# Optimization experiments

Measured on AMD Instinct MI355X. Metric: run time of the kernel, lower is better.

The kernel has to match this reference:

```python
import jax, jax.numpy as jnp
import numpy as np

N_HEAD = 8
EPS = 1e-5


def setup_inputs() -> dict:
    key = jax.random.key(0)
    ks = jax.random.split(key, 8)
    B, Nq, Ns, C, D = 4, 2048, 2048, 256, 256
    k = jax.random.normal(ks[0], (B, Ns, C), dtype=jnp.float32)
    v = jax.random.normal(ks[1], (B, Ns, D), dtype=jnp.float32)
    q = jax.random.normal(ks[2], (B, Nq, C), dtype=jnp.float32)
    idt = jax.random.normal(ks[3], (B, Nq, D), dtype=jnp.float32)
    s_valid_mask = jax.random.randint(ks[4], (B, Ns), 0, 2, dtype=jnp.int32)
    W_qk = jax.random.normal(ks[5], (C, C), dtype=jnp.float32) / np.sqrt(C)
    W_fc = jax.random.normal(ks[6], (D, D), dtype=jnp.float32) / np.sqrt(D)
    b_fc = jnp.zeros((D,), dtype=jnp.float32)
    ln_w = jnp.ones((D,), dtype=jnp.float32)
    ln_b = jnp.zeros((D,), dtype=jnp.float32)
    return {"k": k, "v": v, "q": q, "idt": idt, "s_valid_mask": s_valid_mask,
            "W_qk": W_qk, "W_fc": W_fc, "b_fc": b_fc, "ln_w": ln_w, "ln_b": ln_b}


def reference(k, v, q, idt, s_valid_mask, W_qk, W_fc, b_fc, ln_w, ln_b):
    B, Nq, C = q.shape
    Ns, D = v.shape[1], v.shape[2]
    H = N_HEAD
    hd = C // H
    temp = hd ** (-0.5)
    # shared qk projection (Linear, no bias): y = x @ W^T
    qh = (q @ W_qk.T).reshape(B, Nq, H, hd)  # bqhd
    kh = (k @ W_qk.T).reshape(B, Ns, H, hd)  # bkhd
    vh = v.reshape(B, Ns, H, D // H)         # bkhd (v_fc is Identity)
    scores = jnp.einsum('bqhd,bkhd->bhqk', qh, kh) * temp
    # additive padding mask: masked (==1) positions get -1000
    mask = s_valid_mask.astype(scores.dtype)[:, None, None, :] * (-1000.0)
    attn = jax.nn.softmax(scores + mask, axis=-1)  # (B,H,Nq,Ns)
    out = jnp.einsum('bhqk,bkhd->bqhd', attn, vh).reshape(B, Nq, D)
    out = out @ W_fc.T + b_fc
    x = out + idt
    mu = jnp.mean(x, axis=-1, keepdims=True)
    var = jnp.mean((x - mu) ** 2, axis=-1, keepdims=True)
    out_ln = (x - mu) * jax.lax.rsqrt(var + EPS) * ln_w + ln_b
    return out_ln, attn.reshape(B * H, Nq, Ns)
```

## Files before the change

### kernel.cpp

```cpp
#include <hip/hip_runtime.h>
#include <hip/hip_bf16.h>

typedef __bf16 bf16;
typedef __attribute__((ext_vector_type(8))) __bf16 b16x8;
typedef __attribute__((ext_vector_type(4))) float f32x4;
typedef __attribute__((ext_vector_type(4))) int i32x4;

#define MFMA16(a, b, c) __builtin_amdgcn_mfma_f32_16x16x32_bf16((a), (b), (c), 0, 0, 0)

#define QSCALE 0.25501568077324936f
#define MCONST -1442.6950408889634f

__global__ void __launch_bounds__(256) k_prep(const float* __restrict__ q,
                                              const float* __restrict__ kk,
                                              const float* __restrict__ Wqk,
                                              const float* __restrict__ v,
                                              const float* __restrict__ Wfc,
                                              const int* __restrict__ svalid,
                                              bf16* __restrict__ ph,
                                              bf16* __restrict__ vT,
                                              bf16* __restrict__ Wfcb,
                                              float* __restrict__ maskf) {
    __shared__ __align__(16) char smem[10240];
    int tid = threadIdx.x;
    int idx = blockIdx.x;
    if (idx < 1024) {
        bf16(*sA)[40] = (bf16(*)[40])smem;
        bf16(*sB)[40] = (bf16(*)[40])(smem + 5120);
        int w = tid >> 6, l = tid & 63, lg = l >> 4, ll = l & 15;
        int wm = w >> 1, wn = w & 1;
        int m0 = (idx & 255) * 64, n0 = (idx >> 8) * 64;
        const float* A = (m0 < 8192) ? q + (size_t)m0 * 256 : kk + (size_t)(m0 - 8192) * 256;
        float osc = (m0 < 8192) ? QSCALE : 1.0f;
        f32x4 acc[2][2] = {};
        int ar = tid >> 2, ac = (tid & 3) * 8;
#pragma unroll
        for (int k0 = 0; k0 < 256; k0 += 32) {
            __syncthreads();
            f32x4 a0 = *(const f32x4*)(A + (size_t)ar * 256 + k0 + ac);
            f32x4 a1 = *(const f32x4*)(A + (size_t)ar * 256 + k0 + ac + 4);
            f32x4 b0 = *(const f32x4*)(Wqk + (size_t)(n0 + ar) * 256 + k0 + ac);
            f32x4 b1 = *(const f32x4*)(Wqk + (size_t)(n0 + ar) * 256 + k0 + ac + 4);
            b16x8 av, bv;
#pragma unroll
            for (int i = 0; i < 4; i++) {
                av[i] = (bf16)a0[i]; av[4 + i] = (bf16)a1[i];
                bv[i] = (bf16)b0[i]; bv[4 + i] = (bf16)b1[i];
            }
            *(b16x8*)&sA[ar][ac] = av;
            *(b16x8*)&sB[ar][ac] = bv;
            __syncthreads();
            b16x8 af[2], bfr[2];
#pragma unroll
            for (int f = 0; f < 2; f++) {
                af[f] = *(b16x8*)&sA[wm * 32 + f * 16 + ll][8 * lg];
                bfr[f] = *(b16x8*)&sB[wn * 32 + f * 16 + ll][8 * lg];
            }
#pragma unroll
            for (int i = 0; i < 2; i++)
#pragma unroll
                for (int j = 0; j < 2; j++) acc[i][j] = MFMA16(af[i], bfr[j], acc[i][j]);
        }
#pragma unroll
        for (int i = 0; i < 2; i++)
#pragma unroll
            for (int j = 0; j < 2; j++) {
                int row = m0 + wm * 32 + i * 16 + lg * 4;
                int col = n0 + wn * 32 + j * 16 + ll;
#pragma unroll
                for (int r = 0; r < 4; r++)
                    ph[(size_t)(row + r) * 256 + col] = (bf16)(acc[i][j][r] * osc);
            }
    } else if (idx < 2048) {
        bf16(*sT)[72] = (bf16(*)[72])smem;
        int i2 = idx - 1024;
        int bh = i2 >> 5, b = bh >> 3, h = bh & 7;
        int ns0 = (i2 & 31) * 64;
        int ns = tid >> 2;
        int dp = (tid & 3) * 8;
        const float* sp = v + ((size_t)(b * 2048 + ns0 + ns)) * 256 + h * 32 + dp;
        f32x4 a = *(const f32x4*)sp;
        f32x4 c = *(const f32x4*)(sp + 4);
#pragma unroll
        for (int i = 0; i < 4; i++) sT[dp + i][ns] = (bf16)a[i];
#pragma unroll
        for (int i = 0; i < 4; i++) sT[dp + 4 + i][ns] = (bf16)c[i];
        __syncthreads();
        int d = tid >> 3;
        int nc = (tid & 7) * 8;
        b16x8 o = *(b16x8*)&sT[d][nc];
        *(b16x8*)(vT + ((size_t)bh * 32 + d) * 2048 + ns0 + nc) = o;
    } else if (idx < 2080) {
        int i = (idx - 2048) * 2048 + tid * 8;
        f32x4 a = *(const f32x4*)(Wfc + i);
        f32x4 b = *(const f32x4*)(Wfc + i + 4);
        b16x8 o;
        o[0] = (bf16)a[0]; o[1] = (bf16)a[1]; o[2] = (bf16)a[2]; o[3] = (bf16)a[3];
        o[4] = (bf16)b[0]; o[5] = (bf16)b[1]; o[6] = (bf16)b[2]; o[7] = (bf16)b[3];
        *(b16x8*)(Wfcb + i) = o;
    } else {
#pragma unroll
        for (int c = 0; c < 32; c++) {
            int i = c * 256 + tid;
            maskf[i] = MCONST * (float)svalid[i];
        }
    }
}

__global__ void __launch_bounds__(256) k_attn(const bf16* __restrict__ ph,
                                              const bf16* __restrict__ vT,
                                              const float* __restrict__ maskf,
                                              bf16* __restrict__ xO,
                                              float* __restrict__ attn) {
    __shared__ __align__(16) bf16 sK[64][40];
    __shared__ __align__(16) bf16 sV[32][72];
    __shared__ __align__(16) float sPf[4][16][68];
    int tid = threadIdx.x;
    int w = tid >> 6, l = tid & 63, lg = l >> 4, ll = l & 15;
    int bh = blockIdx.x >> 5, qt = blockIdx.x & 31;
    int b = bh >> 3, h = bh & 7;
    int qrow0 = qt * 64 + w * 16;
    b16x8 qf = *(const b16x8*)(ph + (size_t)(b * 2048 + qrow0 + ll) * 256 + h * 32 + 8 * lg);
    const float* mrow = maskf + b * 2048;
    const bf16* kbase = ph + (size_t)(8192 + b * 2048) * 256 + h * 32;
    const bf16* vbase = vT + (size_t)(bh * 32) * 2048;
    int kr = tid >> 2, kc = (tid & 3) * 8;
    int dr = tid >> 3, nc2 = (tid & 7) * 8;
    float lsum = 0.f;
    {
        *(b16x8*)&sK[kr][kc] = *(const b16x8*)(kbase + (size_t)kr * 256 + kc);
        __syncthreads();
        for (int kt = 0; kt < 2048; kt += 64) {
            bool more = (kt + 64) < 2048;
            b16x8 kst;
            if (more)
                kst = *(const b16x8*)(kbase + (size_t)(kt + 64 + kr) * 256 + kc);
            b16x8 kf[4];
#pragma unroll
            for (int n = 0; n < 4; n++) kf[n] = *(b16x8*)&sK[n * 16 + ll][8 * lg];
            f32x4 s[4];
#pragma unroll
            for (int n = 0; n < 4; n++) {
                f32x4 z = {};
                s[n] = MFMA16(kf[n], qf, z);
            }
#pragma unroll
            for (int n = 0; n < 4; n++) {
                f32x4 mk = *(const f32x4*)&mrow[kt + n * 16 + lg * 4];
#pragma unroll
                for (int r = 0; r < 4; r++) lsum += exp2f(s[n][r] + mk[r]);
            }
            __syncthreads();
            if (more) *(b16x8*)&sK[kr][kc] = kst;
            __syncthreads();
        }
    }
    lsum += __shfl_xor(lsum, 16, 64);
    lsum += __shfl_xor(lsum, 32, 64);
    float linv = 1.f / lsum;
    f32x4 o[2] = {};
    float* outb = attn + (size_t)(bh * 2048 + qrow0) * 2048;
    *(b16x8*)&sK[kr][kc] = *(const b16x8*)(kbase + (size_t)kr * 256 + kc);
    *(b16x8*)&sV[dr][nc2] = *(const b16x8*)(vbase + (size_t)dr * 2048 + nc2);
    __syncthreads();
    for (int kt = 0; kt < 2048; kt += 64) {
        bool more = (kt + 64) < 2048;
        b16x8 kst, vst;
        if (more) {
            kst = *(const b16x8*)(kbase + (size_t)(kt + 64 + kr) * 256 + kc);
            vst = *(const b16x8*)(vbase + (size_t)dr * 2048 + kt + 64 + nc2);
        }
        b16x8 kf[4], vf[2][2];
#pragma unroll
        for (int n = 0; n < 4; n++) kf[n] = *(b16x8*)&sK[n * 16 + ll][8 * lg];
#pragma unroll
        for (int ks = 0; ks < 2; ks++)
#pragma unroll
            for (int j = 0; j < 2; j++)
                vf[ks][j] = *(b16x8*)&sV[j * 16 + ll][ks * 32 + 8 * lg];
        f32x4 s[4];
#pragma unroll
        for (int n = 0; n < 4; n++) {
            f32x4 z = {};
            s[n] = MFMA16(kf[n], qf, z);
        }
#pragma unroll
        for (int n = 0; n < 4; n++) {
            f32x4 mk = *(const f32x4*)&mrow[kt + n * 16 + lg * 4];
            f32x4 ov;
#pragma unroll
            for (int r = 0; r < 4; r++) ov[r] = exp2f(s[n][r] + mk[r]) * linv;
            *(f32x4*)&sPf[w][ll][n * 16 + lg * 4] = ov;
        }
#pragma unroll
        for (int j = 0; j < 4; j++) {
            int row16 = lg + 4 * j;
            f32x4 v = *(f32x4*)&sPf[w][row16][ll * 4];
            __builtin_nontemporal_store(v, (f32x4*)(outb + (size_t)row16 * 2048 + kt + ll * 4));
        }
#pragma unroll
        for (int ks = 0; ks < 2; ks++) {
            f32x4 p0 = *(f32x4*)&sPf[w][ll][ks * 32 + 8 * lg];
            f32x4 p1 = *(f32x4*)&sPf[w][ll][ks * 32 + 8 * lg + 4];
            b16x8 pf;
#pragma unroll
            for (int i = 0; i < 4; i++) {
                pf[i] = (bf16)p0[i];
                pf[4 + i] = (bf16)p1[i];
            }
#pragma unroll
            for (int j = 0; j < 2; j++) o[j] = MFMA16(pf, vf[ks][j], o[j]);
        }
        __syncthreads();
        if (more) {
            *(b16x8*)&sK[kr][kc] = kst;
            *(b16x8*)&sV[dr][nc2] = vst;
        }
        __syncthreads();
    }
#pragma unroll
    for (int r = 0; r < 4; r++) {
        int row = b * 2048 + qrow0 + lg * 4 + r;
#pragma unroll
        for (int j = 0; j < 2; j++) {
            int col = h * 32 + j * 16 + ll;
            xO[(size_t)(row >> 5) * 16384 + (row & 31) * 256 + col] = (bf16)o[j][r];
        }
    }
}

__global__ void __launch_bounds__(256) k_fcln(const bf16* __restrict__ xO,
                                              const bf16* __restrict__ Wfcb,
                                              const float* __restrict__ bias,
                                              const float* __restrict__ idt,
                                              const float* __restrict__ lnw,
                                              const float* __restrict__ lnb,
                                              float* __restrict__ out) {
    __shared__ __align__(16) bf16 sA[32][264];
    __shared__ __align__(16) bf16 sB[256][40];
    __shared__ float sRed[4][32][2];
    int tid = threadIdx.x;
    int w = tid >> 6, l = tid & 63, lg = l >> 4, ll = l & 15;
    int t = blockIdx.x;
#pragma unroll
    for (int c = 0; c < 4; c++) {
        int col = (tid & 7) * 8 + c * 64;
        *(b16x8*)&sA[tid >> 3][col] =
            *(const b16x8*)(xO + (size_t)t * 16384 + (tid >> 3) * 256 + col);
    }
    __syncthreads();
    f32x4 acc[2][4] = {};
#pragma unroll
    for (int k0 = 0; k0 < 256; k0 += 32) {
        if (k0) __syncthreads();
#pragma unroll
        for (int c = 0; c < 4; c++)
            *(b16x8*)&sB[tid][c * 8] = *(const b16x8*)(Wfcb + (size_t)tid * 256 + k0 + c * 8);
        __syncthreads();
        b16x8 af[2];
#pragma unroll
        for (int i = 0; i < 2; i++) af[i] = *(b16x8*)&sA[i * 16 + ll][k0 + 8 * lg];
#pragma unroll
        for (int j = 0; j < 4; j++) {
            b16x8 bfr = *(b16x8*)&sB[w * 64 + j * 16 + ll][8 * lg];
#pragma unroll
            for (int i = 0; i < 2; i++) acc[i][j] = MFMA16(af[i], bfr, acc[i][j]);
        }
    }
    float bcol[4], wcol[4], bbl[4];
#pragma unroll
    for (int j = 0; j < 4; j++) {
        int col = w * 64 + j * 16 + ll;
        bcol[j] = bias[col];
        wcol[j] = lnw[col];
        bbl[j] = lnb[col];
    }
#pragma unroll
    for (int i = 0; i < 2; i++)
#pragma unroll
        for (int r = 0; r < 4; r++) {
            int row32 = i * 16 + lg * 4 + r;
            int grow = t * 32 + row32;
            float a = 0.f, b2 = 0.f;
#pragma unroll
            for (int j = 0; j < 4; j++) {
                float xv = acc[i][j][r] + bcol[j] + idt[(size_t)grow * 256 + w * 64 + j * 16 + ll];
                acc[i][j][r] = xv;
                a += xv;
                b2 += xv * xv;
            }
#pragma unroll
            for (int off = 1; off < 16; off <<= 1) {
                a += __shfl_xor(a, off, 64);
                b2 += __shfl_xor(b2, off, 64);
            }
            if (ll == 0) {
                sRed[w][row32][0] = a;
                sRed[w][row32][1] = b2;
            }
        }
    __syncthreads();
#pragma unroll
    for (int i = 0; i < 2; i++)
#pragma unroll
        for (int r = 0; r < 4; r++) {
            int row32 = i * 16 + lg * 4 + r;
            int grow = t * 32 + row32;
            float st = sRed[0][row32][0] + sRed[1][row32][0] + sRed[2][row32][0] + sRed[3][row32][0];
            float st2 = sRed[0][row32][1] + sRed[1][row32][1] + sRed[2][row32][1] + sRed[3][row32][1];
            float mu = st * (1.f / 256.f);
            float var = st2 * (1.f / 256.f) - mu * mu;
            float rstd = rsqrtf(var + 1e-5f);
#pragma unroll
            for (int j = 0; j < 4; j++)
                out[(size_t)grow * 256 + w * 64 + j * 16 + ll] =
                    (acc[i][j][r] - mu) * rstd * wcol[j] + bbl[j];
        }
}

extern "C" void kernel_launch(void* const* d_in, const int* in_sizes, int n_in,
                              void* d_out, int out_size, void* d_ws, size_t ws_size,
                              hipStream_t stream) {
    const float* k_in = (const float*)d_in[0];
    const float* v_in = (const float*)d_in[1];
    const float* q_in = (const float*)d_in[2];
    const float* idt  = (const float*)d_in[3];
    const int* svalid = (const int*)d_in[4];
    const float* Wqk  = (const float*)d_in[5];
    const float* Wfc  = (const float*)d_in[6];
    const float* bfc  = (const float*)d_in[7];
    const float* lnw  = (const float*)d_in[8];
    const float* lnb  = (const float*)d_in[9];

    float* out_ln = (float*)d_out;
    float* attn = out_ln + 2097152;

    char* ws = (char*)d_ws;
    bf16* ph     = (bf16*)ws;
    bf16* vT     = (bf16*)(ws + 8388608);
    bf16* Wfcb   = (bf16*)(ws + 12582912);
    float* maskf = (float*)(ws + 12713984);

    bf16* xO = (bf16*)out_ln;

    k_prep<<<2081, 256, 0, stream>>>(q_in, k_in, Wqk, v_in, Wfc, svalid, ph, vT, Wfcb, maskf);
    k_attn<<<1024, 256, 0, stream>>>(ph, vT, maskf, xO, attn);
    k_fcln<<<256, 256, 0, stream>>>(xO, Wfcb, bfc, idt, lnw, lnb, out_ln);
}
```

Baseline: 183.2 us.

## Load K and V fragments directly from global into registers, drop LDS staging

The attention kernel stops staging K and V tiles through shared memory. Each wave now loads its own MFMA operand fragments straight from global memory into registers and prefetches the next tile one iteration ahead. This removes both block-wide barriers per iteration and the LDS round trip. In exchange each K/V element is fetched by all four waves instead of once per block, which relies on cache hits, and the extra prefetch registers raise register pressure.

```diff
diff --git a/kernel.cpp b/kernel.cpp
--- a/kernel.cpp
+++ b/kernel.cpp
@@ -112,8 +112,6 @@
                                               const float* __restrict__ maskf,
                                               bf16* __restrict__ xO,
                                               float* __restrict__ attn) {
-    __shared__ __align__(16) bf16 sK[64][40];
-    __shared__ __align__(16) bf16 sV[32][72];
     __shared__ __align__(16) float sPf[4][16][68];
     int tid = threadIdx.x;
     int w = tid >> 6, l = tid & 63, lg = l >> 4, ll = l & 15;
@@ -122,22 +120,21 @@
     int qrow0 = qt * 64 + w * 16;
     b16x8 qf = *(const b16x8*)(ph + (size_t)(b * 2048 + qrow0 + ll) * 256 + h * 32 + 8 * lg);
     const float* mrow = maskf + b * 2048;
-    const bf16* kbase = ph + (size_t)(8192 + b * 2048) * 256 + h * 32;
-    const bf16* vbase = vT + (size_t)(bh * 32) * 2048;
-    int kr = tid >> 2, kc = (tid & 3) * 8;
-    int dr = tid >> 3, nc2 = (tid & 7) * 8;
+    const bf16* kfb = ph + (size_t)(8192 + b * 2048) * 256 + h * 32 + 8 * lg;
+    const bf16* vfb = vT + (size_t)(bh * 32) * 2048 + 8 * lg;
     float lsum = 0.f;
     {
-        *(b16x8*)&sK[kr][kc] = *(const b16x8*)(kbase + (size_t)kr * 256 + kc);
-        __syncthreads();
+        b16x8 kf[4], kn[4];
+#pragma unroll
+        for (int n = 0; n < 4; n++)
+            kf[n] = *(const b16x8*)(kfb + (size_t)(n * 16 + ll) * 256);
         for (int kt = 0; kt < 2048; kt += 64) {
             bool more = (kt + 64) < 2048;
-            b16x8 kst;
-            if (more)
-                kst = *(const b16x8*)(kbase + (size_t)(kt + 64 + kr) * 256 + kc);
-            b16x8 kf[4];
-#pragma unroll
-            for (int n = 0; n < 4; n++) kf[n] = *(b16x8*)&sK[n * 16 + ll][8 * lg];
+            if (more) {
+#pragma unroll
+                for (int n = 0; n < 4; n++)
+                    kn[n] = *(const b16x8*)(kfb + (size_t)(kt + 64 + n * 16 + ll) * 256);
+            }
             f32x4 s[4];
 #pragma unroll
             for (int n = 0; n < 4; n++) {
@@ -150,9 +147,8 @@
 #pragma unroll
                 for (int r = 0; r < 4; r++) lsum += exp2f(s[n][r] + mk[r]);
             }
-            __syncthreads();
-            if (more) *(b16x8*)&sK[kr][kc] = kst;
-            __syncthreads();
+#pragma unroll
+            for (int n = 0; n < 4; n++) kf[n] = kn[n];
         }
     }
     lsum += __shfl_xor(lsum, 16, 64);
@@ -160,24 +156,27 @@
     float linv = 1.f / lsum;
     f32x4 o[2] = {};
     float* outb = attn + (size_t)(bh * 2048 + qrow0) * 2048;
-    *(b16x8*)&sK[kr][kc] = *(const b16x8*)(kbase + (size_t)kr * 256 + kc);
-    *(b16x8*)&sV[dr][nc2] = *(const b16x8*)(vbase + (size_t)dr * 2048 + nc2);
-    __syncthreads();
+    b16x8 kf[4], kn[4], vf[2][2], vn[2][2];
+#pragma unroll
+    for (int n = 0; n < 4; n++)
+        kf[n] = *(const b16x8*)(kfb + (size_t)(n * 16 + ll) * 256);
+#pragma unroll
+    for (int ks = 0; ks < 2; ks++)
+#pragma unroll
+        for (int j = 0; j < 2; j++)
+            vf[ks][j] = *(const b16x8*)(vfb + (size_t)(j * 16 + ll) * 2048 + ks * 32);
     for (int kt = 0; kt < 2048; kt += 64) {
         bool more = (kt + 64) < 2048;
-        b16x8 kst, vst;
         if (more) {
-            kst = *(const b16x8*)(kbase + (size_t)(kt + 64 + kr) * 256 + kc);
-            vst = *(const b16x8*)(vbase + (size_t)dr * 2048 + kt + 64 + nc2);
-        }
-        b16x8 kf[4], vf[2][2];
-#pragma unroll
-        for (int n = 0; n < 4; n++) kf[n] = *(b16x8*)&sK[n * 16 + ll][8 * lg];
-#pragma unroll
-        for (int ks = 0; ks < 2; ks++)
-#pragma unroll
-            for (int j = 0; j < 2; j++)
-                vf[ks][j] = *(b16x8*)&sV[j * 16 + ll][ks * 32 + 8 * lg];
+#pragma unroll
+            for (int n = 0; n < 4; n++)
+                kn[n] = *(const b16x8*)(kfb + (size_t)(kt + 64 + n * 16 + ll) * 256);
+#pragma unroll
+            for (int ks = 0; ks < 2; ks++)
+#pragma unroll
+                for (int j = 0; j < 2; j++)
+                    vn[ks][j] = *(const b16x8*)(vfb + (size_t)(j * 16 + ll) * 2048 + kt + 64 + ks * 32);
+        }
         f32x4 s[4];
 #pragma unroll
         for (int n = 0; n < 4; n++) {
@@ -211,12 +210,14 @@
 #pragma unroll
             for (int j = 0; j < 2; j++) o[j] = MFMA16(pf, vf[ks][j], o[j]);
         }
-        __syncthreads();
         if (more) {
-            *(b16x8*)&sK[kr][kc] = kst;
-            *(b16x8*)&sV[dr][nc2] = vst;
-        }
-        __syncthreads();
+#pragma unroll
+            for (int n = 0; n < 4; n++) kf[n] = kn[n];
+#pragma unroll
+            for (int ks = 0; ks < 2; ks++)
+#pragma unroll
+                for (int j = 0; j < 2; j++) vf[ks][j] = vn[ks][j];
+        }
     }
 #pragma unroll
     for (int r = 0; r < 4; r++) {
```

Measured after the change: 261.4 us. +42.6%, slower.
